# Optimization experiments

Measured on AMD Instinct MI355X. Metric: run time of the kernel, lower is better.

The kernel has to match this reference:

```python
import jax, jax.numpy as jnp
import numpy as np

COST_CLASS, COST_BOX = 1.0, 5.0   # HungarianMatcher defaults
W_CLASS, W_BOX = 1.0, 5.0         # weight_dict
B, Q, M, NUM_CLASSES = 64, 900, 64, 4


def _hungarian(cost):
    """Jonker-Volgenant shortest augmenting path (same optimum as scipy's
    linear_sum_assignment). cost: [n, m] numpy, n <= m. Returns, for each
    row i, the assigned column index."""
    n, m = cost.shape
    u = np.zeros(n + 1, dtype=np.float64)
    v = np.zeros(m + 1, dtype=np.float64)
    p = np.zeros(m + 1, dtype=np.int64)    # p[j]: row matched to col j (1-based), 0=free
    way = np.zeros(m + 1, dtype=np.int64)
    cost = cost.astype(np.float64)
    for i in range(1, n + 1):
        p[0] = i
        j0 = 0
        minv = np.full(m + 1, np.inf)
        used = np.zeros(m + 1, dtype=bool)
        while True:
            used[j0] = True
            i0 = p[j0]
            cur = cost[i0 - 1, :] - u[i0] - v[1:]           # reduced costs, len m
            mask = ~used[1:]
            upd = mask & (cur < minv[1:])
            minv[1:][upd] = cur[upd]
            way[1:][upd] = j0
            cand = np.where(mask, minv[1:], np.inf)
            j1 = int(np.argmin(cand)) + 1
            delta = cand[j1 - 1]
            u[p[used]] += delta
            v[used] -= delta
            minv[1:][mask] -= delta
            j0 = j1
            if p[j0] == 0:
                break
        while j0 != 0:                                       # augment along path
            j1 = way[j0]
            p[j0] = p[j1]
            j0 = j1
    row_to_col = np.zeros(n, dtype=np.int64)
    for j in range(1, m + 1):
        if p[j] > 0:
            row_to_col[p[j] - 1] = j - 1
    return row_to_col


def _match(pred_boxes, pred_classes, gt_boxes, gt_labels, valid):
    """Host-side (no-grad) Hungarian matching, mirroring HungarianMatcher.
    Returns flat (batch_ids, pred_ids, gt_ids) numpy index arrays over all
    matched pairs; gt_ids index into the ORIGINAL [M] gt axis."""
    b_ids, p_ids, g_ids = [], [], []
    for b in range(pred_boxes.shape[0]):
        vpos = np.where(valid[b])[0]
        m = vpos.shape[0]
        if m == 0:
            continue
        logits = pred_classes[b]
        z = logits - logits.max(-1, keepdims=True)
        prob = np.exp(z)
        prob /= prob.sum(-1, keepdims=True)                  # softmax [Q, C]
        labels = gt_labels[b][vpos]
        cost_class = -prob[:, labels]                        # [Q, m]
        gb = gt_boxes[b][vpos]                               # [m, 6]
        cost_box = np.abs(pred_boxes[b][:, None, :] - gb[None, :, :]).sum(-1)  # L1 cdist [Q, m]
        cost = COST_CLASS * cost_class + COST_BOX * cost_box
        pred_idx = _hungarian(cost.T)                        # gt row -> pred col
        b_ids.append(np.full(m, b, dtype=np.int64))
        p_ids.append(pred_idx)
        g_ids.append(vpos.astype(np.int64))
    return (np.concatenate(b_ids), np.concatenate(p_ids), np.concatenate(g_ids))


def setup_inputs() -> dict:
    key = jax.random.key(0)
    k1, k2, k3, k4, k5 = jax.random.split(key, 5)
    return {
        "pred_boxes": jax.random.normal(k1, (B, Q, 6), dtype=jnp.float32),
        "pred_classes": jax.random.normal(k2, (B, Q, NUM_CLASSES), dtype=jnp.float32),
        "gt_boxes": jax.random.normal(k3, (B, M, 6), dtype=jnp.float32),
        "gt_labels": jax.random.randint(k4, (B, M), 0, NUM_CLASSES, dtype=jnp.int64),
        "gt_valid_mask": jax.random.bernoulli(k5, 0.8, (B, M)),
    }


def reference(pred_boxes, pred_classes, gt_boxes, gt_labels, gt_valid_mask):
    b_ids, p_ids, g_ids = _match(
        np.asarray(pred_boxes), np.asarray(pred_classes),
        np.asarray(gt_boxes), np.asarray(gt_labels), np.asarray(gt_valid_mask))
    n = b_ids.shape[0]
    labels = jnp.asarray(gt_labels)[b_ids, g_ids]            # [N]
    # class loss: mean cross-entropy over matched pairs
    logp = jax.nn.log_softmax(pred_classes[b_ids, p_ids], axis=-1)  # [N, C]
    class_loss = -jnp.mean(jnp.take_along_axis(logp, labels[:, None], axis=1))
    # box loss: elementwise-mean L1 over matched pairs
    box_loss = jnp.mean(jnp.abs(pred_boxes[b_ids, p_ids] - gt_boxes[b_ids, g_ids]))
    total_loss = W_CLASS * class_loss + W_BOX * box_loss
    return jnp.stack([class_loss, box_loss, total_loss])
```

## Files before the change

### kernel.cpp

```cpp
#include <hip/hip_runtime.h>
#include <cfloat>
#include <cmath>

#define NB 64
#define NQ 900
#define NM 64
#define NC 4
#define THREADS 256
#define NCT 225

#define S4_LIST(X) X(0) X(1) X(2) X(3)

__device__ __forceinline__ unsigned int uminu(unsigned int a, unsigned int b) {
    return a < b ? a : b;
}

__device__ __forceinline__ unsigned int wave_redmin_u32(unsigned int x) {
    int t;
    t = __builtin_amdgcn_update_dpp(-1, (int)x, 0x111, 0xF, 0xF, false);
    x = uminu(x, (unsigned)t);
    t = __builtin_amdgcn_update_dpp(-1, (int)x, 0x112, 0xF, 0xF, false);
    x = uminu(x, (unsigned)t);
    t = __builtin_amdgcn_update_dpp(-1, (int)x, 0x114, 0xF, 0xF, false);
    x = uminu(x, (unsigned)t);
    t = __builtin_amdgcn_update_dpp(-1, (int)x, 0x118, 0xF, 0xF, false);
    x = uminu(x, (unsigned)t);
    unsigned a = (unsigned)__builtin_amdgcn_readlane((int)x, 15);
    unsigned b = (unsigned)__builtin_amdgcn_readlane((int)x, 31);
    unsigned c = (unsigned)__builtin_amdgcn_readlane((int)x, 47);
    unsigned d = (unsigned)__builtin_amdgcn_readlane((int)x, 63);
    return uminu(uminu(a, b), uminu(c, d));
}

__device__ __forceinline__ void wave_argmin_f(float lmin, int lj,
                                              float& mv, int& mj) {
    unsigned u = __float_as_uint(lmin);
    unsigned key = (u & 0x80000000u) ? ~u : (u | 0x80000000u);
    unsigned mk = wave_redmin_u32(key);
    unsigned long long bal = __ballot(key == mk);
    int fl = (int)__builtin_ctzll(bal);
    mj = __builtin_amdgcn_readlane(lj, fl);
    unsigned mu = (mk & 0x80000000u) ? (mk & 0x7FFFFFFFu) : ~mk;
    mv = __uint_as_float(mu);
}

__global__ __launch_bounds__(THREADS, 1) void match_kernel(
    const float* __restrict__ pred_boxes,
    const float* __restrict__ pred_classes,
    const float* __restrict__ gt_boxes,
    const unsigned int* __restrict__ labels_w,
    const unsigned int* __restrict__ mask_w,
    const unsigned char* __restrict__ mask_b,
    float* __restrict__ cls_part, float* __restrict__ box_part,
    int* __restrict__ cnt_part)
{
    __shared__ float4 pbx4[NQ];
    __shared__ float2 pbx2[NQ];
    __shared__ float  probT[NC][NQ];
    __shared__ int    pcol[NQ + 1];
    __shared__ int    claim[NQ];
    __shared__ int    way_lds[NQ + 1];
    __shared__ float  upot[NM + 1];
    __shared__ float4 gb4[NM];
    __shared__ float2 gb2[NM];
    __shared__ int    lab[NM];
    __shared__ int    vpos_s[NM];
    __shared__ int    row2col[NM];
    __shared__ float  rowmin_s[NM];
    __shared__ int    rowarg_s[NM];
    __shared__ float  rpart_v[4][NM];
    __shared__ int    rpart_j[4][NM];
    __shared__ int    ua_s[NM];
    __shared__ int    nua_s;
    __shared__ int    m_sh;
    __shared__ int    f_lab_odd, f_m_not01, f_m_odd;
    __shared__ __align__(16) float redv[4];
    __shared__ __align__(16) int   redj[4];
    __shared__ float  redc[4], redb[4];

    const int b = blockIdx.x;
    const int tid = threadIdx.x;
    const int lane = tid & 63;
    const int wv = tid >> 6;

    if (tid == 0) { f_lab_odd = 0; f_m_not01 = 0; f_m_odd = 0; }
    __syncthreads();

    for (int w = tid; w < 1024; w += THREADS) {
        unsigned int lw = labels_w[w];
        if ((w & 1) && lw != 0u) f_lab_odd = 1;
        unsigned int mw = mask_w[w];
        if (mw > 1u) f_m_not01 = 1;
        if ((w & 1) && mw != 0u) f_m_odd = 1;
    }
    for (int q = tid; q < NQ; q += THREADS) {
        const float4 lg = *reinterpret_cast<const float4*>(
            pred_classes + ((size_t)b * NQ + q) * NC);
        float mx = fmaxf(fmaxf(lg.x, lg.y), fmaxf(lg.z, lg.w));
        float e0 = expf(lg.x - mx), e1 = expf(lg.y - mx);
        float e2 = expf(lg.z - mx), e3 = expf(lg.w - mx);
        float inv = 1.0f / (e0 + e1 + e2 + e3);
        probT[0][q] = e0 * inv; probT[1][q] = e1 * inv;
        probT[2][q] = e2 * inv; probT[3][q] = e3 * inv;
        const float* bp = pred_boxes + ((size_t)b * NQ + q) * 6;
        float2 b0 = *reinterpret_cast<const float2*>(bp);
        float2 b1 = *reinterpret_cast<const float2*>(bp + 2);
        float2 b2 = *reinterpret_cast<const float2*>(bp + 4);
        pbx4[q] = make_float4(b0.x, b0.y, b1.x, b1.y);
        pbx2[q] = make_float2(b2.x, b2.y);
    }
    for (int j = tid; j <= NQ; j += THREADS) { pcol[j] = 0; way_lds[j] = 0; }
    for (int j = tid; j < NQ; j += THREADS) claim[j] = 0x7FFFFFFF;
    __syncthreads();

    const int lmode = f_lab_odd ? 0 : 1;
    const int mmode = f_m_not01 ? 2 : (f_m_odd ? 0 : 1);

    if (tid < 64) {
        int vv;
        if (mmode == 2)      vv = (mask_b[b * NM + lane] != 0);
        else if (mmode == 1) vv = (mask_w[(b * NM + lane) * 2] != 0u);
        else                 vv = (mask_w[b * NM + lane] != 0u);
        unsigned long long bal = __ballot(vv);
        if (vv) {
            int pos = (int)__popcll(bal & ((1ull << lane) - 1ull));
            vpos_s[pos] = lane;
        }
        if (lane == 0) m_sh = (int)__popcll(bal);
        __builtin_amdgcn_wave_barrier();
        int nw = (int)__popcll(bal);
        if (lane < nw) {
            int g = vpos_s[lane];
            lab[lane] = (int)(lmode ? labels_w[(size_t)(b * NM + g) * 2]
                                    : labels_w[b * NM + g]);
            const float* gp = gt_boxes + ((size_t)b * NM + g) * 6;
            gb4[lane] = make_float4(gp[0], gp[1], gp[2], gp[3]);
            gb2[lane] = make_float2(gp[4], gp[5]);
        }
    }
    __syncthreads();
    const int n = m_sh;

    const bool lv = (tid < NCT);
    const int qb = lv ? (tid << 2) : 0;
#define DECL_COL(s) float cb0_##s, cb1_##s, cb2_##s, cb3_##s, cb4_##s, cb5_##s;
    S4_LIST(DECL_COL)
    float cq0_0, cq0_1, cq0_2, cq0_3;
    float cq1_0, cq1_1, cq1_2, cq1_3;
    float cq2_0, cq2_1, cq2_2, cq2_3;
    float cq3_0, cq3_1, cq3_2, cq3_3;
#define HOIST(s) { const float4 h4 = pbx4[qb + (s)]; \
        const float2 h2 = pbx2[qb + (s)]; \
        cb0_##s = h4.x; cb1_##s = h4.y; cb2_##s = h4.z; cb3_##s = h4.w; \
        cb4_##s = h2.x; cb5_##s = h2.y; }
    S4_LIST(HOIST)
    {
        const float4 p0 = *reinterpret_cast<const float4*>(&probT[0][qb]);
        const float4 p1 = *reinterpret_cast<const float4*>(&probT[1][qb]);
        const float4 p2 = *reinterpret_cast<const float4*>(&probT[2][qb]);
        const float4 p3 = *reinterpret_cast<const float4*>(&probT[3][qb]);
        cq0_0 = p0.x; cq0_1 = p0.y; cq0_2 = p0.z; cq0_3 = p0.w;
        cq1_0 = p1.x; cq1_1 = p1.y; cq1_2 = p1.z; cq1_3 = p1.w;
        cq2_0 = p2.x; cq2_1 = p2.y; cq2_2 = p2.z; cq2_3 = p2.w;
        cq3_0 = p3.x; cq3_1 = p3.y; cq3_2 = p3.z; cq3_3 = p3.w;
    }

    for (int k = 0; k < n; ++k) {
        const float4 g4 = gb4[k];
        const float2 g2 = gb2[k];
        const int lb = lab[k];
        float lmin = FLT_MAX; int lj = NQ + 2;
#define RSCAN(s) { \
        float l1 = fabsf(cb0_##s - g4.x) + fabsf(cb1_##s - g4.y) \
                 + fabsf(cb2_##s - g4.z) + fabsf(cb3_##s - g4.w) \
                 + fabsf(cb4_##s - g2.x) + fabsf(cb5_##s - g2.y); \
        float pr = (lb == 0) ? cq0_##s : ((lb == 1) ? cq1_##s \
                 : ((lb == 2) ? cq2_##s : cq3_##s)); \
        float c = 5.0f * l1 - pr; \
        if (lv && c < lmin) { lmin = c; lj = qb + (s); } }
        S4_LIST(RSCAN)
        float mv; int mj;
        wave_argmin_f(lmin, lj, mv, mj);
        if (lane == 0) { rpart_v[wv][k] = mv; rpart_j[wv][k] = mj; }
    }
    __syncthreads();
    if (tid < n) {
        float bv = rpart_v[0][tid]; int bj = rpart_j[0][tid];
        #pragma unroll
        for (int w = 1; w < 4; ++w) {
            float vw = rpart_v[w][tid]; int jw = rpart_j[w][tid];
            if (vw < bv || (vw == bv && jw < bj)) { bv = vw; bj = jw; }
        }
        rowmin_s[tid] = bv; rowarg_s[tid] = bj;
    }
    __syncthreads();

    if (tid < n) atomicMin(&claim[rowarg_s[tid]], tid);
    for (int k = tid; k < n; k += THREADS) upot[k + 1] = rowmin_s[k];
    if (tid == 0) upot[0] = 0.f;
    __syncthreads();
    if (tid < n) {
        int a = rowarg_s[tid];
        if (claim[a] == tid) pcol[a + 1] = tid + 1;
    }
    if (tid < 64) {
        int un = (lane < n) && (claim[rowarg_s[lane]] != lane);
        unsigned long long bal = __ballot(un);
        if (un) ua_s[(int)__popcll(bal & ((1ull << lane) - 1ull))] = lane;
        if (lane == 0) nua_s = (int)__popcll(bal);
    }
    __syncthreads();

    {
        float minv_0, minv_1, minv_2, minv_3;
        float vpot_0 = 0.f, vpot_1 = 0.f, vpot_2 = 0.f, vpot_3 = 0.f;
        const int nua = nua_s;

        for (int t = 0; t < nua; ++t) {
            const int i = ua_s[t] + 1;
            minv_0 = FLT_MAX; minv_1 = FLT_MAX;
            minv_2 = FLT_MAX; minv_3 = FLT_MAX;
            unsigned int usedm = 0;
            int intree = 0;
            if (tid == 0) pcol[0] = i;
            int j0 = 0, i0 = i, bj = 0;
            __syncthreads();
            while (true) {
                if (j0 > 0 && ((j0 - 1) >> 2) == tid)
                    usedm |= 1u << ((j0 - 1) & 3);
                if (tid == i0 - 1) intree = 1;
                const float base = upot[i0];
                const float4 g4 = gb4[i0 - 1];
                const float2 g2 = gb2[i0 - 1];
                const int lb = lab[i0 - 1];
                float lmin = FLT_MAX; int lj = NQ + 2;
#define SSCAN(s) { \
                float l1 = fabsf(cb0_##s - g4.x) + fabsf(cb1_##s - g4.y) \
                         + fabsf(cb2_##s - g4.z) + fabsf(cb3_##s - g4.w) \
                         + fabsf(cb4_##s - g2.x) + fabsf(cb5_##s - g2.y); \
                float pr = (lb == 0) ? cq0_##s : ((lb == 1) ? cq1_##s \
                         : ((lb == 2) ? cq2_##s : cq3_##s)); \
                float cost = 5.0f * l1 - pr; \
                float cur = cost - base - vpot_##s; \
                if (lv && !((usedm >> (s)) & 1u)) { \
                    if (cur < minv_##s) { minv_##s = cur; \
                                          way_lds[qb + (s) + 1] = j0; } \
                    if (minv_##s < lmin) { lmin = minv_##s; \
                                           lj = qb + (s) + 1; } } }
                S4_LIST(SSCAN)
                float pv; int pj;
                wave_argmin_f(lmin, lj, pv, pj);
                if (lane == 0) { redv[wv] = pv; redj[wv] = pj; }
                __syncthreads();
                const float4 rv4 = *reinterpret_cast<const float4*>(redv);
                const int4   rj4 = *reinterpret_cast<const int4*>(redj);
                float dv = rv4.x; int dj = rj4.x;
                if (rv4.y < dv || (rv4.y == dv && rj4.y < dj)) { dv = rv4.y; dj = rj4.y; }
                if (rv4.z < dv || (rv4.z == dv && rj4.z < dj)) { dv = rv4.z; dj = rj4.z; }
                if (rv4.w < dv || (rv4.w == dv && rj4.w < dj)) { dv = rv4.w; dj = rj4.w; }
                const float delta = dv;
                bj = dj;
                const int nr = pcol[bj];
#define UPDATE(s) { if ((usedm >> (s)) & 1u) vpot_##s -= delta; \
                    else                     minv_##s -= delta; }
                S4_LIST(UPDATE)
                if (intree) upot[tid + 1] += delta;
                __syncthreads();
                if (nr == 0) break;
                j0 = bj; i0 = nr;
            }
            if (tid == 0) {
                int jcur = bj;
                while (jcur != 0) {
                    int jp = way_lds[jcur];
                    pcol[jcur] = pcol[jp];
                    jcur = jp;
                }
            }
        }
    }
    __syncthreads();

    for (int j = 1 + tid; j <= NQ; j += THREADS) {
        int r = pcol[j];
        if (r > 0) row2col[r - 1] = j - 1;
    }
    __syncthreads();
    float cs = 0.f, bs = 0.f;
    for (int k = tid; k < n; k += THREADS) {
        int q = row2col[k];
        int lb = lab[k];
        cs += -logf(probT[lb][q]);
        float4 p4 = pbx4[q]; float2 p2 = pbx2[q];
        float4 g4 = gb4[k];  float2 g2 = gb2[k];
        bs += fabsf(p4.x - g4.x) + fabsf(p4.y - g4.y) + fabsf(p4.z - g4.z)
            + fabsf(p4.w - g4.w) + fabsf(p2.x - g2.x) + fabsf(p2.y - g2.y);
    }
    for (int off = 32; off > 0; off >>= 1) {
        cs += __shfl_down(cs, off);
        bs += __shfl_down(bs, off);
    }
    {
        int wave = tid >> 6;
        if ((tid & 63) == 0) { redc[wave] = cs; redb[wave] = bs; }
    }
    __syncthreads();
    if (tid == 0) {
        cls_part[b] = redc[0] + redc[1] + redc[2] + redc[3];
        box_part[b] = redb[0] + redb[1] + redb[2] + redb[3];
        cnt_part[b] = n;
    }
}

__global__ void finalize_kernel(const float* __restrict__ cls_part,
                                const float* __restrict__ box_part,
                                const int* __restrict__ cnt_part,
                                float* __restrict__ out) {
    if (threadIdx.x == 0 && blockIdx.x == 0) {
        float c = 0.f, bx = 0.f;
        int nn = 0;
        for (int b = 0; b < NB; ++b) {
            c += cls_part[b]; bx += box_part[b]; nn += cnt_part[b];
        }
        float denom = (nn > 0) ? (float)nn : 1.0f;
        float cl = c / denom;
        float bl = bx / (6.0f * denom);
        out[0] = cl;
        out[1] = bl;
        out[2] = cl + 5.0f * bl;
    }
}

extern "C" void kernel_launch(void* const* d_in, const int* in_sizes, int n_in,
                              void* d_out, int out_size, void* d_ws, size_t ws_size,
                              hipStream_t stream) {
    const float* pred_boxes   = (const float*)d_in[0];
    const float* pred_classes = (const float*)d_in[1];
    const float* gt_boxes     = (const float*)d_in[2];
    const unsigned int*  labels_w = (const unsigned int*)d_in[3];
    const unsigned int*  mask_w   = (const unsigned int*)d_in[4];
    const unsigned char* mask_b   = (const unsigned char*)d_in[4];

    char* ws = (char*)d_ws;
    float* cls_part = (float*)(ws + 16);
    float* box_part = (float*)(ws + 16 + 4 * NB);
    int*   cnt_part = (int*)(ws + 16 + 8 * NB);
    float* out = (float*)d_out;

    match_kernel<<<NB, THREADS, 0, stream>>>(pred_boxes, pred_classes, gt_boxes,
                                             labels_w, mask_w, mask_b,
                                             cls_part, box_part, cnt_part);
    finalize_kernel<<<1, 64, 0, stream>>>(cls_part, box_part, cnt_part, out);
}
```

Before: 40.46 us.

## Remove per-iteration barrier in augmenting search via double-buffered reductions

```diff
diff --git a/kernel.cpp b/kernel.cpp
--- a/kernel.cpp
+++ b/kernel.cpp
@@ -74,8 +74,8 @@
     __shared__ int    nua_s;
     __shared__ int    m_sh;
     __shared__ int    f_lab_odd, f_m_not01, f_m_odd;
-    __shared__ __align__(16) float redv[4];
-    __shared__ __align__(16) int   redj[4];
+    __shared__ __align__(16) float redv[2][4];
+    __shared__ __align__(16) int   redj[2][4];
     __shared__ float  redc[4], redb[4];
 
     const int b = blockIdx.x;
@@ -93,28 +93,56 @@
         if (mw > 1u) f_m_not01 = 1;
         if ((w & 1) && mw != 0u) f_m_odd = 1;
     }
-    for (int q = tid; q < NQ; q += THREADS) {
-        const float4 lg = *reinterpret_cast<const float4*>(
-            pred_classes + ((size_t)b * NQ + q) * NC);
-        float mx = fmaxf(fmaxf(lg.x, lg.y), fmaxf(lg.z, lg.w));
-        float e0 = expf(lg.x - mx), e1 = expf(lg.y - mx);
-        float e2 = expf(lg.z - mx), e3 = expf(lg.w - mx);
-        float inv = 1.0f / (e0 + e1 + e2 + e3);
-        probT[0][q] = e0 * inv; probT[1][q] = e1 * inv;
-        probT[2][q] = e2 * inv; probT[3][q] = e3 * inv;
-        const float* bp = pred_boxes + ((size_t)b * NQ + q) * 6;
-        float2 b0 = *reinterpret_cast<const float2*>(bp);
-        float2 b1 = *reinterpret_cast<const float2*>(bp + 2);
-        float2 b2 = *reinterpret_cast<const float2*>(bp + 4);
-        pbx4[q] = make_float4(b0.x, b0.y, b1.x, b1.y);
-        pbx2[q] = make_float2(b2.x, b2.y);
-    }
     for (int j = tid; j <= NQ; j += THREADS) { pcol[j] = 0; way_lds[j] = 0; }
     for (int j = tid; j < NQ; j += THREADS) claim[j] = 0x7FFFFFFF;
     __syncthreads();
 
     const int lmode = f_lab_odd ? 0 : 1;
     const int mmode = f_m_not01 ? 2 : (f_m_odd ? 0 : 1);
+
+    const bool lv = (tid < NCT);
+    const int qb = tid << 2;
+#define DECL_COL(s) float cb0_##s = 0.f, cb1_##s = 0.f, cb2_##s = 0.f, \
+                          cb3_##s = 0.f, cb4_##s = 0.f, cb5_##s = 0.f, \
+                          cq0_##s = 0.f, cq1_##s = 0.f, cq2_##s = 0.f, \
+                          cq3_##s = 0.f;
+    S4_LIST(DECL_COL)
+    if (lv) {
+        const float* cp = pred_classes + ((size_t)b * NQ + qb) * NC;
+        const float4 lg0 = *reinterpret_cast<const float4*>(cp + 0);
+        const float4 lg1 = *reinterpret_cast<const float4*>(cp + 4);
+        const float4 lg2 = *reinterpret_cast<const float4*>(cp + 8);
+        const float4 lg3 = *reinterpret_cast<const float4*>(cp + 12);
+#define SOFTM(s, LG) { \
+        float mx = fmaxf(fmaxf(LG.x, LG.y), fmaxf(LG.z, LG.w)); \
+        float e0 = expf(LG.x - mx), e1 = expf(LG.y - mx); \
+        float e2 = expf(LG.z - mx), e3 = expf(LG.w - mx); \
+        float inv = 1.0f / (e0 + e1 + e2 + e3); \
+        cq0_##s = e0 * inv; cq1_##s = e1 * inv; \
+        cq2_##s = e2 * inv; cq3_##s = e3 * inv; \
+        probT[0][qb + (s)] = cq0_##s; probT[1][qb + (s)] = cq1_##s; \
+        probT[2][qb + (s)] = cq2_##s; probT[3][qb + (s)] = cq3_##s; }
+        SOFTM(0, lg0) SOFTM(1, lg1) SOFTM(2, lg2) SOFTM(3, lg3)
+        const float* bp = pred_boxes + ((size_t)b * NQ + qb) * 6;
+        const float4 b0 = *reinterpret_cast<const float4*>(bp + 0);
+        const float4 b1 = *reinterpret_cast<const float4*>(bp + 4);
+        const float4 b2 = *reinterpret_cast<const float4*>(bp + 8);
+        const float4 b3 = *reinterpret_cast<const float4*>(bp + 12);
+        const float4 b4 = *reinterpret_cast<const float4*>(bp + 16);
+        const float4 b5 = *reinterpret_cast<const float4*>(bp + 20);
+        cb0_0 = b0.x; cb1_0 = b0.y; cb2_0 = b0.z; cb3_0 = b0.w;
+        cb4_0 = b1.x; cb5_0 = b1.y;
+        cb0_1 = b1.z; cb1_1 = b1.w; cb2_1 = b2.x; cb3_1 = b2.y;
+        cb4_1 = b2.z; cb5_1 = b2.w;
+        cb0_2 = b3.x; cb1_2 = b3.y; cb2_2 = b3.z; cb3_2 = b3.w;
+        cb4_2 = b4.x; cb5_2 = b4.y;
+        cb0_3 = b4.z; cb1_3 = b4.w; cb2_3 = b5.x; cb3_3 = b5.y;
+        cb4_3 = b5.z; cb5_3 = b5.w;
+#define STORE_PBX(s) { pbx4[qb + (s)] = make_float4(cb0_##s, cb1_##s, \
+                           cb2_##s, cb3_##s); \
+                       pbx2[qb + (s)] = make_float2(cb4_##s, cb5_##s); }
+        S4_LIST(STORE_PBX)
+    }
 
     if (tid < 64) {
         int vv;
@@ -141,47 +169,43 @@
     __syncthreads();
     const int n = m_sh;
 
-    const bool lv = (tid < NCT);
-    const int qb = lv ? (tid << 2) : 0;
-#define DECL_COL(s) float cb0_##s, cb1_##s, cb2_##s, cb3_##s, cb4_##s, cb5_##s;
-    S4_LIST(DECL_COL)
-    float cq0_0, cq0_1, cq0_2, cq0_3;
-    float cq1_0, cq1_1, cq1_2, cq1_3;
-    float cq2_0, cq2_1, cq2_2, cq2_3;
-    float cq3_0, cq3_1, cq3_2, cq3_3;
-#define HOIST(s) { const float4 h4 = pbx4[qb + (s)]; \
-        const float2 h2 = pbx2[qb + (s)]; \
-        cb0_##s = h4.x; cb1_##s = h4.y; cb2_##s = h4.z; cb3_##s = h4.w; \
-        cb4_##s = h2.x; cb5_##s = h2.y; }
-    S4_LIST(HOIST)
+#define RSCANX(s, G4, G2, LB, LMIN, LJ) { \
+        float l1 = fabsf(cb0_##s - G4.x) + fabsf(cb1_##s - G4.y) \
+                 + fabsf(cb2_##s - G4.z) + fabsf(cb3_##s - G4.w) \
+                 + fabsf(cb4_##s - G2.x) + fabsf(cb5_##s - G2.y); \
+        float pr = ((LB) == 0) ? cq0_##s : (((LB) == 1) ? cq1_##s \
+                 : (((LB) == 2) ? cq2_##s : cq3_##s)); \
+        float c = 5.0f * l1 - pr; \
+        if (lv && c < (LMIN)) { (LMIN) = c; (LJ) = qb + (s); } }
     {
-        const float4 p0 = *reinterpret_cast<const float4*>(&probT[0][qb]);
-        const float4 p1 = *reinterpret_cast<const float4*>(&probT[1][qb]);
-        const float4 p2 = *reinterpret_cast<const float4*>(&probT[2][qb]);
-        const float4 p3 = *reinterpret_cast<const float4*>(&probT[3][qb]);
-        cq0_0 = p0.x; cq0_1 = p0.y; cq0_2 = p0.z; cq0_3 = p0.w;
-        cq1_0 = p1.x; cq1_1 = p1.y; cq1_2 = p1.z; cq1_3 = p1.w;
-        cq2_0 = p2.x; cq2_1 = p2.y; cq2_2 = p2.z; cq2_3 = p2.w;
-        cq3_0 = p3.x; cq3_1 = p3.y; cq3_2 = p3.z; cq3_3 = p3.w;
-    }
-
-    for (int k = 0; k < n; ++k) {
-        const float4 g4 = gb4[k];
-        const float2 g2 = gb2[k];
-        const int lb = lab[k];
-        float lmin = FLT_MAX; int lj = NQ + 2;
-#define RSCAN(s) { \
-        float l1 = fabsf(cb0_##s - g4.x) + fabsf(cb1_##s - g4.y) \
-                 + fabsf(cb2_##s - g4.z) + fabsf(cb3_##s - g4.w) \
-                 + fabsf(cb4_##s - g2.x) + fabsf(cb5_##s - g2.y); \
-        float pr = (lb == 0) ? cq0_##s : ((lb == 1) ? cq1_##s \
-                 : ((lb == 2) ? cq2_##s : cq3_##s)); \
-        float c = 5.0f * l1 - pr; \
-        if (lv && c < lmin) { lmin = c; lj = qb + (s); } }
-        S4_LIST(RSCAN)
-        float mv; int mj;
-        wave_argmin_f(lmin, lj, mv, mj);
-        if (lane == 0) { rpart_v[wv][k] = mv; rpart_j[wv][k] = mj; }
+        int k = 0;
+        for (; k + 1 < n; k += 2) {
+            const float4 g4a = gb4[k];     const float2 g2a = gb2[k];
+            const int lba = lab[k];
+            const float4 g4b = gb4[k + 1]; const float2 g2b = gb2[k + 1];
+            const int lbb = lab[k + 1];
+            float lmina = FLT_MAX; int lja = NQ + 2;
+            float lminb = FLT_MAX; int ljb = NQ + 2;
+#define RSA(s) RSCANX(s, g4a, g2a, lba, lmina, lja)
+#define RSB(s) RSCANX(s, g4b, g2b, lbb, lminb, ljb)
+            S4_LIST(RSA) S4_LIST(RSB)
+            float mva, mvb; int mja, mjb;
+            wave_argmin_f(lmina, lja, mva, mja);
+            wave_argmin_f(lminb, ljb, mvb, mjb);
+            if (lane == 0) {
+                rpart_v[wv][k] = mva;     rpart_j[wv][k] = mja;
+                rpart_v[wv][k + 1] = mvb; rpart_j[wv][k + 1] = mjb;
+            }
+        }
+        if (k < n) {
+            const float4 g4a = gb4[k]; const float2 g2a = gb2[k];
+            const int lba = lab[k];
+            float lmina = FLT_MAX; int lja = NQ + 2;
+            S4_LIST(RSA)
+            float mva; int mja;
+            wave_argmin_f(lmina, lja, mva, mja);
+            if (lane == 0) { rpart_v[wv][k] = mva; rpart_j[wv][k] = mja; }
+        }
     }
     __syncthreads();
     if (tid < n) {
@@ -223,16 +247,16 @@
             unsigned int usedm = 0;
             int intree = 0;
             if (tid == 0) pcol[0] = i;
-            int j0 = 0, i0 = i, bj = 0;
             __syncthreads();
+            float base = upot[i];
+            float4 g4 = gb4[i - 1];
+            float2 g2 = gb2[i - 1];
+            int lb = lab[i - 1];
+            int j0 = 0, i0 = i, bj = 0, par = 0;
             while (true) {
                 if (j0 > 0 && ((j0 - 1) >> 2) == tid)
                     usedm |= 1u << ((j0 - 1) & 3);
                 if (tid == i0 - 1) intree = 1;
-                const float base = upot[i0];
-                const float4 g4 = gb4[i0 - 1];
-                const float2 g2 = gb2[i0 - 1];
-                const int lb = lab[i0 - 1];
                 float lmin = FLT_MAX; int lj = NQ + 2;
 #define SSCAN(s) { \
                 float l1 = fabsf(cb0_##s - g4.x) + fabsf(cb1_##s - g4.y) \
@@ -250,10 +274,10 @@
                 S4_LIST(SSCAN)
                 float pv; int pj;
                 wave_argmin_f(lmin, lj, pv, pj);
-                if (lane == 0) { redv[wv] = pv; redj[wv] = pj; }
+                if (lane == 0) { redv[par][wv] = pv; redj[par][wv] = pj; }
                 __syncthreads();
-                const float4 rv4 = *reinterpret_cast<const float4*>(redv);
-                const int4   rj4 = *reinterpret_cast<const int4*>(redj);
+                const float4 rv4 = *reinterpret_cast<const float4*>(redv[par]);
+                const int4   rj4 = *reinterpret_cast<const int4*>(redj[par]);
                 float dv = rv4.x; int dj = rj4.x;
                 if (rv4.y < dv || (rv4.y == dv && rj4.y < dj)) { dv = rv4.y; dj = rj4.y; }
                 if (rv4.z < dv || (rv4.z == dv && rj4.z < dj)) { dv = rv4.z; dj = rj4.z; }
@@ -265,10 +289,14 @@
                     else                     minv_##s -= delta; }
                 S4_LIST(UPDATE)
                 if (intree) upot[tid + 1] += delta;
-                __syncthreads();
                 if (nr == 0) break;
-                j0 = bj; i0 = nr;
+                base = upot[nr];
+                g4 = gb4[nr - 1];
+                g2 = gb2[nr - 1];
+                lb = lab[nr - 1];
+                j0 = bj; i0 = nr; par ^= 1;
             }
+            __syncthreads();
             if (tid == 0) {
                 int jcur = bj;
                 while (jcur != 0) {
```

Result: no change. 39.73 us (-1.8%).
